# Kernel optimization log

Hardware: AMD Instinct MI355X
Metric: run time of the kernel (lower is better)

Reference implementation:

```python
import jax, jax.numpy as jnp
import numpy as np

N_NODES = 100000
N_EDGES = 1600000
N_GRAPHS = 2048
D = 128
H = 128
EPS = 1e-5


def gcn_conv(x, src, dst, W, b, n):
    # x: [N, Din], W: [Din, Dout]; GCN with added self-loops and symmetric norm
    xw = x @ W                                       # [N, Dout]
    deg = jnp.zeros((n,), x.dtype).at[dst].add(1.0) + 1.0  # deg of A+I (counted on dst)
    dinv = jax.lax.rsqrt(deg)                        # [N]
    norm = dinv[src] * dinv[dst]                     # [E]
    msg = xw[src] * norm[:, None]                    # [E, Dout] gather + scale
    agg = jax.ops.segment_sum(msg, dst, num_segments=n)
    agg = agg + xw * (dinv * dinv)[:, None]          # self-loop contribution
    return agg + b


def gru_step_h0(x, W_ih, W_hh, b_ih, b_hh):
    # single GRU step with h0 = 0 (PyTorch gate order r, z, n)
    h0 = jnp.zeros_like(x)
    gi = x @ W_ih.T + b_ih                           # [G, 3H]
    gh = h0 @ W_hh.T + b_hh                          # [G, 3H] (zeros + b_hh)
    ir, iz, inn = jnp.split(gi, 3, axis=-1)
    hr, hz, hn = jnp.split(gh, 3, axis=-1)
    r = jax.nn.sigmoid(ir + hr)
    z = jax.nn.sigmoid(iz + hz)
    n = jnp.tanh(inn + r * hn)
    return (1.0 - z) * n + z * h0


def setup_inputs() -> dict:
    key = jax.random.key(0)
    ks = jax.random.split(key, 10)
    x = jax.random.normal(ks[0], (N_NODES, D), jnp.float32)
    edge_index = jax.random.randint(ks[1], (2, N_EDGES), 0, N_NODES, jnp.int32)
    batch = jnp.sort(jax.random.randint(ks[2], (N_NODES,), 0, N_GRAPHS, jnp.int32))
    s = 1.0 / np.sqrt(H)
    return {
        "x": x,
        "edge_index": edge_index,
        "batch": batch,
        "W1": jax.random.normal(ks[3], (D, H), jnp.float32) * s,
        "b1": jnp.zeros((H,), jnp.float32),
        "W2": jax.random.normal(ks[4], (H, H), jnp.float32) * s,
        "b2": jnp.zeros((H,), jnp.float32),
        "W_ih": jax.random.normal(ks[5], (3 * H, H), jnp.float32) * s,
        "W_hh": jax.random.normal(ks[6], (3 * H, H), jnp.float32) * s,
        "b_ih": jnp.zeros((3 * H,), jnp.float32),
        "b_hh": jnp.zeros((3 * H,), jnp.float32),
        "W_lin": jax.random.normal(ks[7], (1, H), jnp.float32) * s,
        "b_lin": jnp.zeros((1,), jnp.float32),
    }


def reference(x, edge_index, batch, W1, b1, W2, b2, W_ih, W_hh, b_ih, b_hh, W_lin, b_lin):
    src, dst = edge_index[0], edge_index[1]
    n = x.shape[0]
    h = jax.nn.relu(gcn_conv(x, src, dst, W1, b1, n))
    h = gcn_conv(h, src, dst, W2, b2, n)
    # global_mean_pool over graph ids
    sums = jax.ops.segment_sum(h, batch, num_segments=N_GRAPHS)
    cnts = jax.ops.segment_sum(jnp.ones((n,), h.dtype), batch, num_segments=N_GRAPHS)
    g = sums / jnp.maximum(cnts, 1.0)[:, None]       # [G, H]
    # dropout p=0.5 in eval mode -> identity
    g = gru_step_h0(g, W_ih, W_hh, b_ih, b_hh)
    g = jax.nn.relu(g)
    mu = jnp.mean(g, axis=-1, keepdims=True)
    var = jnp.mean(jnp.square(g - mu), axis=-1, keepdims=True)
    g = (g - mu) * jax.lax.rsqrt(var + EPS)          # layer_norm, no affine
    return g @ W_lin.T + b_lin                       # [G, 1]
```

## Files before the change

### kernel.cpp

```cpp
#include <hip/hip_runtime.h>
#include <hip/hip_bf16.h>
#include <math.h>

#define DHID 128
#define SH 8
#define BIN_T 8192
#define CAPSH 13
#define SRC_SH 13

typedef __attribute__((ext_vector_type(8))) short bf16x8;
typedef __attribute__((ext_vector_type(4))) float f32x4;

__device__ __forceinline__ int atomAddI(int* p, int v) {
    return __hip_atomic_fetch_add(p, v, __ATOMIC_RELAXED, __HIP_MEMORY_SCOPE_AGENT);
}
__device__ __forceinline__ float bf_lo(unsigned u) { return __uint_as_float(u << 16); }
__device__ __forceinline__ float bf_hi(unsigned u) { return __uint_as_float(u & 0xffff0000u); }
__device__ __forceinline__ float bf_us(unsigned short u) { return __uint_as_float((unsigned)u << 16); }
__device__ __forceinline__ unsigned short bf16_1(float f) {
    unsigned u = __float_as_uint(f);
    u += 0x7fffu + ((u >> 16) & 1u);
    return (unsigned short)(u >> 16);
}
__device__ __forceinline__ unsigned pack_bf16x2(float a, float b) {
    unsigned ua = __float_as_uint(a);
    unsigned ub = __float_as_uint(b);
    ua = (ua + 0x7fffu + ((ua >> 16) & 1u)) >> 16;
    ub = (ub + 0x7fffu + ((ub >> 16) & 1u)) & 0xffff0000u;
    return ua | ub;
}

__global__ __launch_bounds__(256) void bin_edges(const int* __restrict__ src,
                                                 const int* __restrict__ dst,
                                                 int* __restrict__ bcur,
                                                 unsigned* __restrict__ staged,
                                                 const float* __restrict__ W1,
                                                 const float* __restrict__ W2,
                                                 const float* __restrict__ Wih,
                                                 unsigned short* __restrict__ Wt1,
                                                 unsigned short* __restrict__ Wt2,
                                                 unsigned short* __restrict__ Wihb,
                                                 int E, int NB, int nb_bin) {
    int t = threadIdx.x;
    if (blockIdx.x >= nb_bin) {
        int idx = (blockIdx.x - nb_bin) * 256 + t;
        if (idx < 16384) {
            int k = idx >> 7, n = idx & 127;
            Wt1[n * 128 + k] = bf16_1(W1[idx]);
        } else if (idx < 32768) {
            int j = idx - 16384;
            int k = j >> 7, n = j & 127;
            Wt2[n * 128 + k] = bf16_1(W2[j]);
        } else if (idx < 32768 + 49152) {
            int j = idx - 32768;
            Wihb[j] = bf16_1(Wih[j]);
        }
        return;
    }
    __shared__ int lh[512], lbase[512], lcur[512];
    int e0 = blockIdx.x * BIN_T;
    int eend = min(e0 + BIN_T, E);
    for (int i = t; i < NB; i += 256) { lh[i] = 0; lcur[i] = 0; }
    __syncthreads();
    for (int e = e0 + t; e < eend; e += 256)
        atomicAdd(&lh[dst[e] >> SH], 1);
    __syncthreads();
    for (int i = t; i < NB; i += 256)
        lbase[i] = lh[i] ? atomAddI(&bcur[i], lh[i]) : 0;
    __syncthreads();
    for (int e = e0 + t; e < eend; e += 256) {
        int d = dst[e];
        int b = d >> SH;
        int pos = lbase[b] + atomicAdd(&lcur[b], 1);
        staged[((size_t)b << CAPSH) + pos] =
            (unsigned)src[e] | ((unsigned)(d & ((1 << SH) - 1)) << 24);
    }
}

__global__ __launch_bounds__(256) void scatter_gemm(const unsigned* __restrict__ staged,
                                                    const int* __restrict__ bcur,
                                                    int* __restrict__ off,
                                                    float* __restrict__ dinv,
                                                    int* __restrict__ rec,
                                                    int N, int E, int NB,
                                                    const float* __restrict__ Xf,
                                                    const unsigned short* __restrict__ Wt,
                                                    unsigned short* __restrict__ Y) {
    __shared__ __align__(16) unsigned char smem[52224];
    const int tid = threadIdx.x;
    if (blockIdx.x < NB) {
        int* hist = (int*)smem;
        int* sh   = (int*)(smem + 16384);
        int t = tid;
        int b = blockIdx.x;
        int node0 = b << SH;

        int s0 = (t < b) ? bcur[t] : 0;
        int s1 = (256 + t < b) ? bcur[256 + t] : 0;
        int s = s0 + s1;
#pragma unroll
        for (int o = 1; o < 64; o <<= 1) s += __shfl_xor(s, o);
        if ((t & 63) == 0) sh[t >> 6] = s;
        __syncthreads();
        int base = sh[0] + sh[1] + sh[2] + sh[3];
        __syncthreads();

        for (int i = t; i < 4096; i += 256) hist[i] = 0;
        __syncthreads();
        int cnt_b = bcur[b];
        const unsigned* st = staged + ((size_t)b << CAPSH);
        for (int j = t; j < cnt_b; j += 256) {
            unsigned w = st[j];
            int key = (int)((w >> 24) << 4) | (int)((w & 0xFFFFFFu) >> SRC_SH);
            atomicAdd(&hist[key], 1);
        }
        __syncthreads();

        int loc[16];
        int run = 0;
        int base16 = t * 16;
#pragma unroll
        for (int i = 0; i < 16; i++) { loc[i] = run; run += hist[base16 + i]; }
        sh[t] = run;
        __syncthreads();
#pragma unroll
        for (int o = 1; o < 256; o <<= 1) {
            int x = (t >= o) ? sh[t - o] : 0;
            __syncthreads();
            sh[t] += x;
            __syncthreads();
        }
        int excl = sh[t] - run;
#pragma unroll
        for (int i = 0; i < 16; i++) hist[base16 + i] = base + excl + loc[i];

        int node = node0 + t;
        if (node < N) {
            off[node] = base + excl;
            dinv[node] = rsqrtf((float)run + 1.0f);
        }
        if (b == NB - 1 && t == 0) off[N] = E;
        __syncthreads();

        for (int j = t; j < cnt_b; j += 256) {
            unsigned w = st[j];
            int key = (int)((w >> 24) << 4) | (int)((w & 0xFFFFFFu) >> SRC_SH);
            int pos = atomicAdd(&hist[key], 1);
            rec[pos] = (int)(w & 0xFFFFFFu);
        }
    } else {
        unsigned short* Xs = (unsigned short*)smem;
        unsigned short* Ws = (unsigned short*)(smem + 17408);
        {
            const uint4* W4 = (const uint4*)Wt;
#pragma unroll
            for (int i = 0; i < 8; i++) {
                int idx = tid + i * 256;
                int r = idx >> 4, c8 = idx & 15;
                *(uint4*)&Ws[r * 136 + c8 * 8] = W4[idx];
            }
        }
        const int row0 = (blockIdx.x - NB) * 64;
        {
            const float4* X4 = (const float4*)Xf;
#pragma unroll
            for (int i = 0; i < 8; i++) {
                int idx = tid + i * 256;
                int r = idx >> 5, c4 = idx & 31;
                float4 v = make_float4(0.f, 0.f, 0.f, 0.f);
                if (row0 + r < N) v = X4[(size_t)(row0 + r) * 32 + c4];
                uint2 pk = make_uint2(pack_bf16x2(v.x, v.y), pack_bf16x2(v.z, v.w));
                *(uint2*)&Xs[r * 136 + c4 * 4] = pk;
            }
        }
        __syncthreads();

        const int lane = tid & 63;
        const int wv = tid >> 6;
        const int m = lane & 15, quad = lane >> 4;
        const int wrow = wv * 16;

        f32x4 acc[8];
#pragma unroll
        for (int i = 0; i < 8; i++) acc[i] = (f32x4){0.f, 0.f, 0.f, 0.f};

#pragma unroll
        for (int kc = 0; kc < 4; kc++) {
            bf16x8 a = *(const bf16x8*)&Xs[(wrow + m) * 136 + kc * 32 + quad * 8];
#pragma unroll
            for (int nt = 0; nt < 8; nt++) {
                bf16x8 bfr = *(const bf16x8*)&Ws[(nt * 16 + m) * 136 + kc * 32 + quad * 8];
                acc[nt] = __builtin_amdgcn_mfma_f32_16x16x32_bf16(a, bfr, acc[nt], 0, 0, 0);
            }
        }

#pragma unroll
        for (int r = 0; r < 4; r++) {
            int lrow = wrow + quad * 4 + r;
#pragma unroll
            for (int nt = 0; nt < 8; nt++)
                Xs[lrow * 136 + nt * 16 + m] = bf16_1(acc[nt][r]);
        }
        __syncthreads();
#pragma unroll
        for (int i = 0; i < 4; i++) {
            int idx = tid + i * 256;
            int r = idx >> 4, c8 = idx & 15;
            if (row0 + r < N)
                *(uint4*)&Y[(size_t)(row0 + r) * DHID + c8 * 8] =
                    *(const uint4*)&Xs[r * 136 + c8 * 8];
        }
    }
}

__global__ __launch_bounds__(256) void aggregate(const unsigned short* __restrict__ A,
                                                 const float* __restrict__ dinv,
                                                 const int* __restrict__ off,
                                                 const int* __restrict__ rec,
                                                 const float* __restrict__ bias,
                                                 unsigned short* __restrict__ Bout,
                                                 int N, int mode) {
    int node = blockIdx.x * 4 + (threadIdx.x >> 6);
    if (node >= N) return;
    int lane = threadIdx.x & 63;
    int q  = lane >> 4;
    int ql = lane & 15;
    float di = dinv[node];
    float2 acc[4];
    if (q == 0) {
        float s = di * di;
        uint4 v = ((const uint4*)(A + (size_t)node * DHID))[ql];
        const float4* bb = (const float4*)(bias + ql * 8);
        float4 b0 = bb[0], b1 = bb[1];
        acc[0] = make_float2(bf_lo(v.x) * s + b0.x, bf_hi(v.x) * s + b0.y);
        acc[1] = make_float2(bf_lo(v.y) * s + b0.z, bf_hi(v.y) * s + b0.w);
        acc[2] = make_float2(bf_lo(v.z) * s + b1.x, bf_hi(v.z) * s + b1.y);
        acc[3] = make_float2(bf_lo(v.w) * s + b1.z, bf_hi(v.w) * s + b1.w);
    } else {
#pragma unroll
        for (int i = 0; i < 4; i++) acc[i] = make_float2(0.f, 0.f);
    }
    int j = off[node] + q;
    int jend = off[node + 1];
    for (; j + 12 < jend; j += 16) {
        int s0 = rec[j], s1 = rec[j + 4], s2 = rec[j + 8], s3 = rec[j + 12];
        uint4 v0 = ((const uint4*)(A + (size_t)s0 * DHID))[ql];
        uint4 v1 = ((const uint4*)(A + (size_t)s1 * DHID))[ql];
        uint4 v2 = ((const uint4*)(A + (size_t)s2 * DHID))[ql];
        uint4 v3 = ((const uint4*)(A + (size_t)s3 * DHID))[ql];
        float w0 = dinv[s0] * di;
        float w1 = dinv[s1] * di;
        float w2 = dinv[s2] * di;
        float w3 = dinv[s3] * di;
        acc[0].x += bf_lo(v0.x) * w0 + bf_lo(v1.x) * w1 + bf_lo(v2.x) * w2 + bf_lo(v3.x) * w3;
        acc[0].y += bf_hi(v0.x) * w0 + bf_hi(v1.x) * w1 + bf_hi(v2.x) * w2 + bf_hi(v3.x) * w3;
        acc[1].x += bf_lo(v0.y) * w0 + bf_lo(v1.y) * w1 + bf_lo(v2.y) * w2 + bf_lo(v3.y) * w3;
        acc[1].y += bf_hi(v0.y) * w0 + bf_hi(v1.y) * w1 + bf_hi(v2.y) * w2 + bf_hi(v3.y) * w3;
        acc[2].x += bf_lo(v0.z) * w0 + bf_lo(v1.z) * w1 + bf_lo(v2.z) * w2 + bf_lo(v3.z) * w3;
        acc[2].y += bf_hi(v0.z) * w0 + bf_hi(v1.z) * w1 + bf_hi(v2.z) * w2 + bf_hi(v3.z) * w3;
        acc[3].x += bf_lo(v0.w) * w0 + bf_lo(v1.w) * w1 + bf_lo(v2.w) * w2 + bf_lo(v3.w) * w3;
        acc[3].y += bf_hi(v0.w) * w0 + bf_hi(v1.w) * w1 + bf_hi(v2.w) * w2 + bf_hi(v3.w) * w3;
    }
    for (; j + 4 < jend; j += 8) {
        int s0 = rec[j], s1 = rec[j + 4];
        uint4 v0 = ((const uint4*)(A + (size_t)s0 * DHID))[ql];
        uint4 v1 = ((const uint4*)(A + (size_t)s1 * DHID))[ql];
        float w0 = dinv[s0] * di;
        float w1 = dinv[s1] * di;
        acc[0].x += bf_lo(v0.x) * w0 + bf_lo(v1.x) * w1;
        acc[0].y += bf_hi(v0.x) * w0 + bf_hi(v1.x) * w1;
        acc[1].x += bf_lo(v0.y) * w0 + bf_lo(v1.y) * w1;
        acc[1].y += bf_hi(v0.y) * w0 + bf_hi(v1.y) * w1;
        acc[2].x += bf_lo(v0.z) * w0 + bf_lo(v1.z) * w1;
        acc[2].y += bf_hi(v0.z) * w0 + bf_hi(v1.z) * w1;
        acc[3].x += bf_lo(v0.w) * w0 + bf_lo(v1.w) * w1;
        acc[3].y += bf_hi(v0.w) * w0 + bf_hi(v1.w) * w1;
    }
    if (j < jend) {
        int s0 = rec[j];
        uint4 v0 = ((const uint4*)(A + (size_t)s0 * DHID))[ql];
        float w0 = dinv[s0] * di;
        acc[0].x += bf_lo(v0.x) * w0;
        acc[0].y += bf_hi(v0.x) * w0;
        acc[1].x += bf_lo(v0.y) * w0;
        acc[1].y += bf_hi(v0.y) * w0;
        acc[2].x += bf_lo(v0.z) * w0;
        acc[2].y += bf_hi(v0.z) * w0;
        acc[3].x += bf_lo(v0.w) * w0;
        acc[3].y += bf_hi(v0.w) * w0;
    }
#pragma unroll
    for (int i = 0; i < 4; i++) {
        acc[i].x += __shfl_xor(acc[i].x, 16);
        acc[i].y += __shfl_xor(acc[i].y, 16);
        acc[i].x += __shfl_xor(acc[i].x, 32);
        acc[i].y += __shfl_xor(acc[i].y, 32);
    }
    if (q == 0) {
        if (mode == 1) {
#pragma unroll
            for (int i = 0; i < 4; i++) {
                acc[i].x = fmaxf(acc[i].x, 0.f);
                acc[i].y = fmaxf(acc[i].y, 0.f);
            }
        }
        uint4 pk;
        pk.x = pack_bf16x2(acc[0].x, acc[0].y);
        pk.y = pack_bf16x2(acc[1].x, acc[1].y);
        pk.z = pack_bf16x2(acc[2].x, acc[2].y);
        pk.w = pack_bf16x2(acc[3].x, acc[3].y);
        ((uint4*)(Bout + (size_t)node * DHID))[ql] = pk;
    }
}

__global__ __launch_bounds__(256) void gemm_mfma(const void* __restrict__ Xv,
                                                 const unsigned short* __restrict__ Wt,
                                                 unsigned short* __restrict__ Y,
                                                 int N, int x_is_bf16,
                                                 int wstride, int ystride) {
    __shared__ unsigned short Xs[64 * 136];
    __shared__ unsigned short Ws[128 * 136];
    const int tid = threadIdx.x;
    const unsigned short* Wg = Wt + (size_t)blockIdx.y * wstride;
    unsigned short* Yg = Y + (size_t)blockIdx.y * ystride;

    {
        const uint4* W4 = (const uint4*)Wg;
#pragma unroll
        for (int i = 0; i < 8; i++) {
            int idx = tid + i * 256;
            int r = idx >> 4, c8 = idx & 15;
            *(uint4*)&Ws[r * 136 + c8 * 8] = W4[idx];
        }
    }
    const int row0 = blockIdx.x * 64;
    if (x_is_bf16) {
        const uint4* X4 = (const uint4*)Xv;
#pragma unroll
        for (int i = 0; i < 4; i++) {
            int idx = tid + i * 256;
            int r = idx >> 4, c8 = idx & 15;
            uint4 v = make_uint4(0u, 0u, 0u, 0u);
            if (row0 + r < N) v = X4[(size_t)(row0 + r) * 16 + c8];
            *(uint4*)&Xs[r * 136 + c8 * 8] = v;
        }
    } else {
        const float4* X4 = (const float4*)Xv;
#pragma unroll
        for (int i = 0; i < 8; i++) {
            int idx = tid + i * 256;
            int r = idx >> 5, c4 = idx & 31;
            float4 v = make_float4(0.f, 0.f, 0.f, 0.f);
            if (row0 + r < N) v = X4[(size_t)(row0 + r) * 32 + c4];
            uint2 pk = make_uint2(pack_bf16x2(v.x, v.y), pack_bf16x2(v.z, v.w));
            *(uint2*)&Xs[r * 136 + c4 * 4] = pk;
        }
    }
    __syncthreads();

    const int lane = tid & 63;
    const int wv = tid >> 6;
    const int m = lane & 15, quad = lane >> 4;
    const int wrow = wv * 16;

    f32x4 acc[8];
#pragma unroll
    for (int i = 0; i < 8; i++) acc[i] = (f32x4){0.f, 0.f, 0.f, 0.f};

#pragma unroll
    for (int kc = 0; kc < 4; kc++) {
        bf16x8 a = *(const bf16x8*)&Xs[(wrow + m) * 136 + kc * 32 + quad * 8];
#pragma unroll
        for (int nt = 0; nt < 8; nt++) {
            bf16x8 b = *(const bf16x8*)&Ws[(nt * 16 + m) * 136 + kc * 32 + quad * 8];
            acc[nt] = __builtin_amdgcn_mfma_f32_16x16x32_bf16(a, b, acc[nt], 0, 0, 0);
        }
    }

#pragma unroll
    for (int r = 0; r < 4; r++) {
        int lrow = wrow + quad * 4 + r;
#pragma unroll
        for (int nt = 0; nt < 8; nt++)
            Xs[lrow * 136 + nt * 16 + m] = bf16_1(acc[nt][r]);
    }
    __syncthreads();
#pragma unroll
    for (int i = 0; i < 4; i++) {
        int idx = tid + i * 256;
        int r = idx >> 4, c8 = idx & 15;
        if (row0 + r < N)
            *(uint4*)&Yg[(size_t)(row0 + r) * DHID + c8 * 8] =
                *(const uint4*)&Xs[r * 136 + c8 * 8];
    }
}

__global__ __launch_bounds__(256) void pool_mean(const unsigned short* __restrict__ B,
                                                 const int* __restrict__ batch,
                                                 float* __restrict__ g, int N, int G) {
    __shared__ int se[2];
    __shared__ float red[128];
    const int t = threadIdx.x;
    const int gr = blockIdx.x;
    if (t < 2) {
        int target = gr + t, lo = 0, hi = N;
        while (lo < hi) {
            int mid = (lo + hi) >> 1;
            if (batch[mid] < target) lo = mid + 1; else hi = mid;
        }
        se[t] = lo;
    }
    __syncthreads();
    const int s = se[0], e = se[1];
    const int col = t & 127, rh = t >> 7;
    float sum = 0.f;
    for (int r = s + rh; r < e; r += 2) sum += bf_us(B[(size_t)r * DHID + col]);
    if (rh == 1) red[col] = sum;
    __syncthreads();
    if (rh == 0) {
        float tot = sum + red[col];
        g[(size_t)gr * DHID + col] = tot / fmaxf((float)(e - s), 1.0f);
    }
}

__global__ __launch_bounds__(128) void gate_ln_head(const unsigned short* __restrict__ gi,
                                                    const float* __restrict__ b_ih,
                                                    const float* __restrict__ b_hh,
                                                    const float* __restrict__ W_lin,
                                                    const float* __restrict__ b_lin,
                                                    float* __restrict__ out, int G) {
    __shared__ float red[2];
    const int t = threadIdx.x;
    const int g = blockIdx.x;

    float d0 = bf_us(gi[(size_t)g * DHID + t]);
    float d1 = bf_us(gi[(size_t)(G + g) * DHID + t]);
    float d2 = bf_us(gi[(size_t)(2 * G + g) * DHID + t]);

    float rg = 1.f / (1.f + expf(-(d0 + b_ih[t] + b_hh[t])));
    float zg = 1.f / (1.f + expf(-(d1 + b_ih[128 + t] + b_hh[128 + t])));
    float ng = tanhf(d2 + b_ih[256 + t] + rg * b_hh[256 + t]);
    float y = fmaxf((1.f - zg) * ng, 0.f);

    auto blockSum = [&](float v) -> float {
#pragma unroll
        for (int o = 1; o < 64; o <<= 1) v += __shfl_xor(v, o);
        __syncthreads();
        if ((t & 63) == 0) red[t >> 6] = v;
        __syncthreads();
        return red[0] + red[1];
    };

    float mu = blockSum(y) * (1.f / 128.f);
    float dy = y - mu;
    float var = blockSum(dy * dy) * (1.f / 128.f);
    float yn = dy * rsqrtf(var + 1e-5f);
    float tot = blockSum(yn * W_lin[t]);
    if (t == 0) out[g] = tot + b_lin[0];
}

extern "C" void kernel_launch(void* const* d_in, const int* in_sizes, int n_in,
                              void* d_out, int out_size, void* d_ws, size_t ws_size,
                              hipStream_t stream) {
    const float* x     = (const float*)d_in[0];
    const int*   ei    = (const int*)d_in[1];
    const int*   batch = (const int*)d_in[2];
    const float* W1    = (const float*)d_in[3];
    const float* b1    = (const float*)d_in[4];
    const float* W2    = (const float*)d_in[5];
    const float* b2    = (const float*)d_in[6];
    const float* W_ih  = (const float*)d_in[7];
    const float* b_ih  = (const float*)d_in[9];
    const float* b_hh  = (const float*)d_in[10];
    const float* W_lin = (const float*)d_in[11];
    const float* b_lin = (const float*)d_in[12];
    float* out = (float*)d_out;

    const int N = in_sizes[0] / DHID;
    const int E = in_sizes[1] / 2;
    const int G = out_size;
    const int* src = ei;
    const int* dst = ei + E;
    const int NB = (N + (1 << SH) - 1) >> SH;

    auto align256 = [](size_t v) { return (v + 255) & ~(size_t)255; };
    char* p = (char*)d_ws;
    size_t used = 0;
    auto carve = [&](size_t bytes) -> char* {
        char* q = p + used;
        used += align256(bytes);
        return q;
    };

    int*   off    = (int*)carve(((size_t)N + 1) * 4);
    int*   bcur   = (int*)carve(512 * 4);
    float* dinv   = (float*)carve((size_t)N * 4);
    unsigned* staged = (unsigned*)carve(((size_t)NB << CAPSH) * 4);
    int*   rec    = (int*)carve((size_t)E * 4);
    float* gbuf   = (float*)carve((size_t)G * DHID * 4);
    unsigned short* Wt1  = (unsigned short*)carve((size_t)128 * 128 * 2);
    unsigned short* Wt2  = (unsigned short*)carve((size_t)128 * 128 * 2);
    unsigned short* Wihb = (unsigned short*)carve((size_t)3 * 128 * 128 * 2);
    unsigned short* gib  = (unsigned short*)carve((size_t)3 * G * DHID * 2);
    unsigned short* A    = (unsigned short*)carve((size_t)N * DHID * 2);
    unsigned short* B1b  = (unsigned short*)carve((size_t)N * DHID * 2);
    size_t matB = (size_t)N * DHID * 2;
    unsigned short* B2b;
    if (ws_size >= used + matB) {
        B2b = (unsigned short*)carve(matB);
    } else {
        B2b = (unsigned short*)d_in[0];
    }

    dim3 blk(256);
    int nb_g  = (N + 63) / 64;
    int nb_ag = (N + 3) / 4;
    int nb_bin = (E + BIN_T - 1) / BIN_T;
    int nb_wp  = (81920 + 255) / 256;

    hipMemsetAsync(bcur, 0, (size_t)NB * 4, stream);
    bin_edges<<<nb_bin + nb_wp, blk, 0, stream>>>(src, dst, bcur, staged,
                                                  W1, W2, W_ih, Wt1, Wt2, Wihb,
                                                  E, NB, nb_bin);
    scatter_gemm<<<NB + nb_g, blk, 0, stream>>>(staged, bcur, off, dinv, rec,
                                                N, E, NB, x, Wt1, A);

    aggregate<<<nb_ag, blk, 0, stream>>>(A, dinv, off, rec, b1, B1b, N, 1);

    gemm_mfma<<<dim3(nb_g, 1), blk, 0, stream>>>(B1b, Wt2, A, N, 1, 0, 0);
    aggregate<<<nb_ag, blk, 0, stream>>>(A, dinv, off, rec, b2, B2b, N, 0);

    pool_mean<<<G, blk, 0, stream>>>(B2b, batch, gbuf, N, G);
    gemm_mfma<<<dim3((G + 63) / 64, 3), blk, 0, stream>>>(gbuf, Wihb, gib, G, 0,
                                                          128 * 128, G * DHID);
    gate_ln_head<<<G, dim3(128), 0, stream>>>(gib, b_ih, b_hh, W_lin, b_lin, out, G);
}
```

Measured before the change: 336.8 us.

## Fuse pooling, GRU input GEMM and LN head into one kernel; prefetch aggregate indices

After: 341.0 us. Within noise of the previous version (+1.3%).

```diff
diff --git a/kernel.cpp b/kernel.cpp
--- a/kernel.cpp
+++ b/kernel.cpp
@@ -242,39 +242,39 @@
     }
     int j = off[node] + q;
     int jend = off[node + 1];
-    for (; j + 12 < jend; j += 16) {
-        int s0 = rec[j], s1 = rec[j + 4], s2 = rec[j + 8], s3 = rec[j + 12];
-        uint4 v0 = ((const uint4*)(A + (size_t)s0 * DHID))[ql];
-        uint4 v1 = ((const uint4*)(A + (size_t)s1 * DHID))[ql];
-        uint4 v2 = ((const uint4*)(A + (size_t)s2 * DHID))[ql];
-        uint4 v3 = ((const uint4*)(A + (size_t)s3 * DHID))[ql];
-        float w0 = dinv[s0] * di;
-        float w1 = dinv[s1] * di;
-        float w2 = dinv[s2] * di;
-        float w3 = dinv[s3] * di;
-        acc[0].x += bf_lo(v0.x) * w0 + bf_lo(v1.x) * w1 + bf_lo(v2.x) * w2 + bf_lo(v3.x) * w3;
-        acc[0].y += bf_hi(v0.x) * w0 + bf_hi(v1.x) * w1 + bf_hi(v2.x) * w2 + bf_hi(v3.x) * w3;
-        acc[1].x += bf_lo(v0.y) * w0 + bf_lo(v1.y) * w1 + bf_lo(v2.y) * w2 + bf_lo(v3.y) * w3;
-        acc[1].y += bf_hi(v0.y) * w0 + bf_hi(v1.y) * w1 + bf_hi(v2.y) * w2 + bf_hi(v3.y) * w3;
-        acc[2].x += bf_lo(v0.z) * w0 + bf_lo(v1.z) * w1 + bf_lo(v2.z) * w2 + bf_lo(v3.z) * w3;
-        acc[2].y += bf_hi(v0.z) * w0 + bf_hi(v1.z) * w1 + bf_hi(v2.z) * w2 + bf_hi(v3.z) * w3;
-        acc[3].x += bf_lo(v0.w) * w0 + bf_lo(v1.w) * w1 + bf_lo(v2.w) * w2 + bf_lo(v3.w) * w3;
-        acc[3].y += bf_hi(v0.w) * w0 + bf_hi(v1.w) * w1 + bf_hi(v2.w) * w2 + bf_hi(v3.w) * w3;
-    }
-    for (; j + 4 < jend; j += 8) {
+    if (j + 4 < jend) {
         int s0 = rec[j], s1 = rec[j + 4];
-        uint4 v0 = ((const uint4*)(A + (size_t)s0 * DHID))[ql];
-        uint4 v1 = ((const uint4*)(A + (size_t)s1 * DHID))[ql];
-        float w0 = dinv[s0] * di;
-        float w1 = dinv[s1] * di;
-        acc[0].x += bf_lo(v0.x) * w0 + bf_lo(v1.x) * w1;
-        acc[0].y += bf_hi(v0.x) * w0 + bf_hi(v1.x) * w1;
-        acc[1].x += bf_lo(v0.y) * w0 + bf_lo(v1.y) * w1;
-        acc[1].y += bf_hi(v0.y) * w0 + bf_hi(v1.y) * w1;
-        acc[2].x += bf_lo(v0.z) * w0 + bf_lo(v1.z) * w1;
-        acc[2].y += bf_hi(v0.z) * w0 + bf_hi(v1.z) * w1;
-        acc[3].x += bf_lo(v0.w) * w0 + bf_lo(v1.w) * w1;
-        acc[3].y += bf_hi(v0.w) * w0 + bf_hi(v1.w) * w1;
+        for (; j + 12 < jend; j += 8) {
+            int n0 = rec[j + 8], n1 = rec[j + 12];
+            uint4 v0 = ((const uint4*)(A + (size_t)s0 * DHID))[ql];
+            uint4 v1 = ((const uint4*)(A + (size_t)s1 * DHID))[ql];
+            float w0 = dinv[s0] * di;
+            float w1 = dinv[s1] * di;
+            acc[0].x += bf_lo(v0.x) * w0 + bf_lo(v1.x) * w1;
+            acc[0].y += bf_hi(v0.x) * w0 + bf_hi(v1.x) * w1;
+            acc[1].x += bf_lo(v0.y) * w0 + bf_lo(v1.y) * w1;
+            acc[1].y += bf_hi(v0.y) * w0 + bf_hi(v1.y) * w1;
+            acc[2].x += bf_lo(v0.z) * w0 + bf_lo(v1.z) * w1;
+            acc[2].y += bf_hi(v0.z) * w0 + bf_hi(v1.z) * w1;
+            acc[3].x += bf_lo(v0.w) * w0 + bf_lo(v1.w) * w1;
+            acc[3].y += bf_hi(v0.w) * w0 + bf_hi(v1.w) * w1;
+            s0 = n0; s1 = n1;
+        }
+        {
+            uint4 v0 = ((const uint4*)(A + (size_t)s0 * DHID))[ql];
+            uint4 v1 = ((const uint4*)(A + (size_t)s1 * DHID))[ql];
+            float w0 = dinv[s0] * di;
+            float w1 = dinv[s1] * di;
+            acc[0].x += bf_lo(v0.x) * w0 + bf_lo(v1.x) * w1;
+            acc[0].y += bf_hi(v0.x) * w0 + bf_hi(v1.x) * w1;
+            acc[1].x += bf_lo(v0.y) * w0 + bf_lo(v1.y) * w1;
+            acc[1].y += bf_hi(v0.y) * w0 + bf_hi(v1.y) * w1;
+            acc[2].x += bf_lo(v0.z) * w0 + bf_lo(v1.z) * w1;
+            acc[2].y += bf_hi(v0.z) * w0 + bf_hi(v1.z) * w1;
+            acc[3].x += bf_lo(v0.w) * w0 + bf_lo(v1.w) * w1;
+            acc[3].y += bf_hi(v0.w) * w0 + bf_hi(v1.w) * w1;
+            j += 8;
+        }
     }
     if (j < jend) {
         int s0 = rec[j];
@@ -395,15 +395,24 @@
     }
 }
 
-__global__ __launch_bounds__(256) void pool_mean(const unsigned short* __restrict__ B,
+__global__ __launch_bounds__(256) void tail_head(const unsigned short* __restrict__ B,
                                                  const int* __restrict__ batch,
-                                                 float* __restrict__ g, int N, int G) {
+                                                 const unsigned short* __restrict__ Wihb,
+                                                 const float* __restrict__ b_ih,
+                                                 const float* __restrict__ b_hh,
+                                                 const float* __restrict__ W_lin,
+                                                 const float* __restrict__ b_lin,
+                                                 float* __restrict__ out,
+                                                 int N, int G) {
+    __shared__ float grow[128];
+    __shared__ float psum[4][128];
+    __shared__ float gi[384];
+    __shared__ float red[4];
     __shared__ int se[2];
-    __shared__ float red[128];
     const int t = threadIdx.x;
-    const int gr = blockIdx.x;
+    const int g = blockIdx.x;
     if (t < 2) {
-        int target = gr + t, lo = 0, hi = N;
+        int target = g + t, lo = 0, hi = N;
         while (lo < hi) {
             int mid = (lo + hi) >> 1;
             if (batch[mid] < target) lo = mid + 1; else hi = mid;
@@ -412,50 +421,75 @@
     }
     __syncthreads();
     const int s = se[0], e = se[1];
-    const int col = t & 127, rh = t >> 7;
-    float sum = 0.f;
-    for (int r = s + rh; r < e; r += 2) sum += bf_us(B[(size_t)r * DHID + col]);
-    if (rh == 1) red[col] = sum;
-    __syncthreads();
-    if (rh == 0) {
-        float tot = sum + red[col];
-        g[(size_t)gr * DHID + col] = tot / fmaxf((float)(e - s), 1.0f);
-    }
-}
-
-__global__ __launch_bounds__(128) void gate_ln_head(const unsigned short* __restrict__ gi,
-                                                    const float* __restrict__ b_ih,
-                                                    const float* __restrict__ b_hh,
-                                                    const float* __restrict__ W_lin,
-                                                    const float* __restrict__ b_lin,
-                                                    float* __restrict__ out, int G) {
-    __shared__ float red[2];
-    const int t = threadIdx.x;
-    const int g = blockIdx.x;
-
-    float d0 = bf_us(gi[(size_t)g * DHID + t]);
-    float d1 = bf_us(gi[(size_t)(G + g) * DHID + t]);
-    float d2 = bf_us(gi[(size_t)(2 * G + g) * DHID + t]);
-
-    float rg = 1.f / (1.f + expf(-(d0 + b_ih[t] + b_hh[t])));
-    float zg = 1.f / (1.f + expf(-(d1 + b_ih[128 + t] + b_hh[128 + t])));
-    float ng = tanhf(d2 + b_ih[256 + t] + rg * b_hh[256 + t]);
-    float y = fmaxf((1.f - zg) * ng, 0.f);
-
+
+    const int c2 = t & 63;
+    const int rh = t >> 6;
+    float sx = 0.f, sy = 0.f;
+    for (int r = s + rh; r < e; r += 4) {
+        unsigned u = *(const unsigned*)(B + (size_t)r * DHID + c2 * 2);
+        sx += bf_lo(u);
+        sy += bf_hi(u);
+    }
+    *(float2*)&psum[rh][c2 * 2] = make_float2(sx, sy);
+    __syncthreads();
+    if (t < 128) {
+        grow[t] = (psum[0][t] + psum[1][t] + psum[2][t] + psum[3][t]) /
+                  fmaxf((float)(e - s), 1.0f);
+    }
+    __syncthreads();
+
+    {
+        float a0 = 0.f;
+        const uint4* wr = (const uint4*)(Wihb + (size_t)t * DHID);
+#pragma unroll
+        for (int k8 = 0; k8 < 16; k8++) {
+            uint4 wv = wr[k8];
+            const float* gk = &grow[k8 * 8];
+            a0 += bf_lo(wv.x) * gk[0] + bf_hi(wv.x) * gk[1]
+                + bf_lo(wv.y) * gk[2] + bf_hi(wv.y) * gk[3]
+                + bf_lo(wv.z) * gk[4] + bf_hi(wv.z) * gk[5]
+                + bf_lo(wv.w) * gk[6] + bf_hi(wv.w) * gk[7];
+        }
+        gi[t] = a0;
+    }
+    if (t < 128) {
+        float a1 = 0.f;
+        const uint4* wr = (const uint4*)(Wihb + (size_t)(256 + t) * DHID);
+#pragma unroll
+        for (int k8 = 0; k8 < 16; k8++) {
+            uint4 wv = wr[k8];
+            const float* gk = &grow[k8 * 8];
+            a1 += bf_lo(wv.x) * gk[0] + bf_hi(wv.x) * gk[1]
+                + bf_lo(wv.y) * gk[2] + bf_hi(wv.y) * gk[3]
+                + bf_lo(wv.z) * gk[4] + bf_hi(wv.z) * gk[5]
+                + bf_lo(wv.w) * gk[6] + bf_hi(wv.w) * gk[7];
+        }
+        gi[256 + t] = a1;
+    }
+    __syncthreads();
+
+    float y = 0.f, wl = 0.f;
+    if (t < 128) {
+        float d0 = gi[t], d1 = gi[128 + t], d2 = gi[256 + t];
+        float rg = 1.f / (1.f + expf(-(d0 + b_ih[t] + b_hh[t])));
+        float zg = 1.f / (1.f + expf(-(d1 + b_ih[128 + t] + b_hh[128 + t])));
+        float ng = tanhf(d2 + b_ih[256 + t] + rg * b_hh[256 + t]);
+        y = fmaxf((1.f - zg) * ng, 0.f);
+        wl = W_lin[t];
+    }
     auto blockSum = [&](float v) -> float {
 #pragma unroll
         for (int o = 1; o < 64; o <<= 1) v += __shfl_xor(v, o);
         __syncthreads();
         if ((t & 63) == 0) red[t >> 6] = v;
         __syncthreads();
-        return red[0] + red[1];
+        return red[0] + red[1] + red[2] + red[3];
     };
-
     float mu = blockSum(y) * (1.f / 128.f);
-    float dy = y - mu;
+    float dy = (t < 128) ? (y - mu) : 0.f;
     float var = blockSum(dy * dy) * (1.f / 128.f);
     float yn = dy * rsqrtf(var + 1e-5f);
-    float tot = blockSum(yn * W_lin[t]);
+    float tot = blockSum(yn * wl);
     if (t == 0) out[g] = tot + b_lin[0];
 }
 
@@ -497,11 +531,9 @@
     float* dinv   = (float*)carve((size_t)N * 4);
     unsigned* staged = (unsigned*)carve(((size_t)NB << CAPSH) * 4);
     int*   rec    = (int*)carve((size_t)E * 4);
-    float* gbuf   = (float*)carve((size_t)G * DHID * 4);
     unsigned short* Wt1  = (unsigned short*)carve((size_t)128 * 128 * 2);
     unsigned short* Wt2  = (unsigned short*)carve((size_t)128 * 128 * 2);
     unsigned short* Wihb = (unsigned short*)carve((size_t)3 * 128 * 128 * 2);
-    unsigned short* gib  = (unsigned short*)carve((size_t)3 * G * DHID * 2);
     unsigned short* A    = (unsigned short*)carve((size_t)N * DHID * 2);
     unsigned short* B1b  = (unsigned short*)carve((size_t)N * DHID * 2);
     size_t matB = (size_t)N * DHID * 2;
@@ -530,8 +562,6 @@
     gemm_mfma<<<dim3(nb_g, 1), blk, 0, stream>>>(B1b, Wt2, A, N, 1, 0, 0);
     aggregate<<<nb_ag, blk, 0, stream>>>(A, dinv, off, rec, b2, B2b, N, 0);
 
-    pool_mean<<<G, blk, 0, stream>>>(B2b, batch, gbuf, N, G);
-    gemm_mfma<<<dim3((G + 63) / 64, 3), blk, 0, stream>>>(gbuf, Wihb, gib, G, 0,
-                                                          128 * 128, G * DHID);
-    gate_ln_head<<<G, dim3(128), 0, stream>>>(gib, b_ih, b_hh, W_lin, b_lin, out, G);
-}
+    tail_head<<<G, blk, 0, stream>>>(B2b, batch, Wihb, b_ih, b_hh, W_lin, b_lin,
+                                     out, N, G);
+}
```
